# Kernel optimization log

Hardware: AMD Instinct MI355X
Metric: run time of the kernel (lower is better)

Reference implementation:

```python
import jax, jax.numpy as jnp
import numpy as np

B, K, V, D, H, S, KS = 4, 4, 32, 64, 4, 1024, 5
GROUPS = K * V  # 128


def setup_inputs() -> dict:
    key = jax.random.key(0)
    k1, k2 = jax.random.split(key, 2)
    x = jax.random.normal(k1, (B, GROUPS * 3, S), dtype=jnp.float32)
    # grouped causal conv weight: (out_ch, in_ch_per_group, ks) = (K*V*D*3, 3, KS)
    W = jax.random.normal(k2, (GROUPS * D * 3, 3, KS), dtype=jnp.float32) * 0.05
    b = jnp.zeros((GROUPS * D * 3,), dtype=jnp.float32)
    return {"x": x, "W": W, "b": b}


def reference(x, W, b):
    temperature = 1.0
    dk = D // H
    # --- TCN (stand-in): causal grouped conv1d, groups = K*V ---
    xp = jnp.pad(x, ((0, 0), (0, 0), (KS - 1, 0)))  # left-pad for causality
    y = jax.lax.conv_general_dilated(
        xp, W, window_strides=(1,), padding='VALID',
        dimension_numbers=('NCH', 'OIH', 'NCH'),
        feature_group_count=GROUPS,
    ) + b[None, :, None]                      # (B, K*V*3*D, S)
    # channel layout per group is (3, D) to mirror torch reshape
    y = y.reshape(B * K, V, 3, D, S)
    q, k, v = y[:, :, 0], y[:, :, 1], y[:, :, 2]   # each (BK, V, D, S)
    q = q.reshape(B * K, V, H, dk, S)
    k = k.reshape(B * K, V, H, dk, S)
    v = v.reshape(B * K, V, H, dk, S)
    scale = (dk ** -0.5) / temperature
    # per-timestep attention over variables: (BK, H, S, Vq, Vk)
    logits = jnp.einsum('bqhds,bkhds->bhsqk', q, k) * scale
    attn = jax.nn.softmax(logits, axis=-1)
    # x_out[b,h,s,q,d] = sum_k attn * v  -> permute(0,3,1,4,2) layout (BK,V,H,dk,S)
    xo = jnp.einsum('bhsqk,bkhds->bqhds', attn, v)
    xo = xo.reshape(B * K, V * D, S).reshape(B, K * V * D, S)
    # mean over heads, to (BK, Vq, Vk, S) then (B, K, V, V, S)
    attn_m = jnp.transpose(attn.mean(axis=1), (0, 2, 3, 1)).reshape(B, K, V, V, S)
    return xo, attn_m
```

## Files before the change

kernel.cpp:

```cpp
#include <hip/hip_runtime.h>
#include <hip/hip_bf16.h>
#include <stdint.h>

#define SCALE 0.25f

typedef __attribute__((ext_vector_type(8))) short bf16x8;
typedef __attribute__((ext_vector_type(4))) float f32x4;
typedef __attribute__((ext_vector_type(16))) float f32x16;

__global__ __launch_bounds__(256) void prep_w2_kernel(const float* __restrict__ W,
                                                      float* __restrict__ W2) {
    int idx = blockIdx.x * 256 + threadIdx.x;
    int o = idx >> 4, j = idx & 15;
    W2[idx] = (j < 15) ? W[o * 15 + j] : 0.f;
}

#define XS_OFF 0
#define QK0_OFF 6912
#define QK1_OFF 23296
#define VT0_OFF 39680
#define VT1_OFF 49920
#define PT_OFF 60160
#define RING_OFF 80640
#define LDS_TOTAL 162880

__global__ __launch_bounds__(512) void fused4_kernel(const float* __restrict__ x,
                                                     const float* __restrict__ W2,
                                                     const float* __restrict__ bias,
                                                     float* __restrict__ out,
                                                     float* __restrict__ out_am) {
    extern __shared__ char smraw[];
    _Float16* xs = (_Float16*)(smraw + XS_OFF);
    unsigned short* pT = (unsigned short*)(smraw + PT_OFF);
    float* xo = (float*)(smraw + RING_OFF);
    float* att = (float*)smraw;

    int bi = blockIdx.x, slot = bi & 7, jj = bi >> 3;
    int k_ = slot >> 1, b = jj >> 4, st = ((slot & 1) << 4) | (jj & 15);
    int bk = b * 4 + k_;

    int t = threadIdx.x;
    int wid = t >> 6, lane = t & 63;
    int l31 = lane & 31, hi2 = lane >> 5;
    int l15 = lane & 15, hi4 = lane >> 4;

    int v = t >> 4, dk = t & 15;
    int g3 = (k_ * 32 + v) * 3;

    float w[3][16], bs[3];
    auto loadw = [&](int hh) {
        #pragma unroll
        for (int c3 = 0; c3 < 3; ++c3) {
            int row = (g3 + c3) * 64 + hh * 16 + dk;
            const float4* p = (const float4*)(W2 + (size_t)row * 16);
            float4 a0 = p[0], a1 = p[1], a2 = p[2], a3 = p[3];
            w[c3][0] = a0.x;  w[c3][1] = a0.y;  w[c3][2] = a0.z;  w[c3][3] = a0.w;
            w[c3][4] = a1.x;  w[c3][5] = a1.y;  w[c3][6] = a1.z;  w[c3][7] = a1.w;
            w[c3][8] = a2.x;  w[c3][9] = a2.y;  w[c3][10] = a2.z; w[c3][11] = a2.w;
            w[c3][12] = a3.x; w[c3][13] = a3.y; w[c3][14] = a3.z; w[c3][15] = a3.w;
            bs[c3] = bias[row];
        }
    };

    auto conv_stage = [&](int qs, int bufi) {
        __hip_bfloat16* qk = (__hip_bfloat16*)(smraw + (bufi ? QK1_OFF : QK0_OFF));
        __hip_bfloat16* vt = (__hip_bfloat16*)(smraw + (bufi ? VT1_OFF : VT0_OFF));
        float xw[3][12];
        #pragma unroll
        for (int i = 0; i < 3; ++i)
            #pragma unroll
            for (int j = 0; j < 12; ++j)
                xw[i][j] = (float)xs[(v * 3 + i) * 36 + qs * 8 + j];
        #pragma unroll
        for (int s8 = 0; s8 < 8; ++s8) {
            float a0 = bs[0], a1 = bs[1], a2 = bs[2];
            #pragma unroll
            for (int i = 0; i < 3; ++i)
                #pragma unroll
                for (int tt = 0; tt < 5; ++tt) {
                    float xv = xw[i][s8 + tt];
                    a0 = fmaf(xv, w[0][i * 5 + tt], a0);
                    a1 = fmaf(xv, w[1][i * 5 + tt], a1);
                    a2 = fmaf(xv, w[2][i * 5 + tt], a2);
                }
            qk[(s8 * 2 + 0) * 512 + v * 16 + dk] = __float2bfloat16(a0);
            qk[(s8 * 2 + 1) * 512 + v * 16 + dk] = __float2bfloat16(a1);
            vt[(s8 * 16 + dk) * 40 + v] = __float2bfloat16(a2);
        }
    };

    auto sweep = [&](int hp) {
        int rb = (32 * hp) % 40;
        int u = t >> 3;
        int s4 = (t & 7) * 4;
        #pragma unroll
        for (int j = 0; j < 8; ++j) {
            int c_loc = j * 64 + u;
            int col = c_loc ^ (4 * ((c_loc >> 4) & 7));
            float4 o;
            #pragma unroll
            for (int i2 = 0; i2 < 4; ++i2) {
                int r = rb + s4 + i2; if (r >= 40) r -= 40;
                (&o.x)[i2] = xo[r * 514 + col];
            }
            int qv = c_loc >> 4, dkc = c_loc & 15;
            int c = k_ * 2048 + qv * 64 + hp * 16 + dkc;
            *(float4*)(out + ((size_t)b * 8192 + c) * 1024 + st * 32 + s4) = o;
        }
    };

    float acc_am[4][16];
    #pragma unroll
    for (int a = 0; a < 4; ++a)
        #pragma unroll
        for (int r = 0; r < 16; ++r) acc_am[a][r] = 0.f;

    loadw(0);
    {
        int sbase = st * 32 - 4;
        #pragma unroll
        for (int i = 0; i < 7; ++i) {
            int idx = i * 512 + t;
            if (idx < 3456) {
                int row = idx / 36, col = idx - row * 36;
                int sg = sbase + col;
                float val = (sg >= 0) ? x[((size_t)b * 384 + k_ * 96 + row) * 1024 + sg] : 0.f;
                xs[idx] = (_Float16)val;
            }
        }
    }
    __syncthreads();
    conv_stage(0, 0);
    __syncthreads();

    for (int h = 0; h < 4; ++h) {
        #pragma unroll
        for (int q = 0; q < 4; ++q) {
            if (q == 3 && h < 3) loadw(h + 1);

            {
                const __hip_bfloat16* qk =
                    (const __hip_bfloat16*)(smraw + ((q & 1) ? QK1_OFF : QK0_OFF));
                const __hip_bfloat16* vt =
                    (const __hip_bfloat16*)(smraw + ((q & 1) ? VT1_OFF : VT0_OFF));
                const __hip_bfloat16* qb = qk + (wid * 2) * 512 + l31 * 16 + hi2 * 8;
                bf16x8 qf = *(const bf16x8*)qb;
                bf16x8 kf = *(const bf16x8*)(qb + 512);

                f32x16 zc;
                #pragma unroll
                for (int i = 0; i < 16; ++i) zc[i] = 0.f;
                f32x16 lg = __builtin_amdgcn_mfma_f32_32x32x16_bf16(kf, qf, zc, 0, 0, 0);

                float p[16], m = -3.0e38f;
                #pragma unroll
                for (int r = 0; r < 16; ++r) { p[r] = lg[r] * SCALE; m = fmaxf(m, p[r]); }
                m = fmaxf(m, __shfl_xor(m, 32));
                float ssum = 0.f;
                #pragma unroll
                for (int r = 0; r < 16; ++r) { p[r] = __expf(p[r] - m); ssum += p[r]; }
                ssum += __shfl_xor(ssum, 32);
                float inv = 1.f / ssum;
                #pragma unroll
                for (int r = 0; r < 16; ++r) { p[r] *= inv; acc_am[q][r] += p[r]; }

                unsigned* pTrow = (unsigned*)(pT + (size_t)(wid * 32 + l31) * 40);
                int wsw = (l31 >> 3) & 1 ? 4 : 0;
                #pragma unroll
                for (int mm = 0; mm < 8; ++mm) {
                    unsigned pk;
                    asm("v_cvt_pk_bf16_f32 %0, %1, %2"
                        : "=v"(pk) : "v"(p[2 * mm]), "v"(p[2 * mm + 1]));
                    pTrow[((mm & 1) + 4 * (mm >> 1) + 2 * hi2) ^ wsw] = pk;
                }

                int rsw = (l15 >> 3) & 1 ? 8 : 0;
                bf16x8 vf = *(const bf16x8*)&vt[(wid * 16 + l15) * 40 + hi4 * 8];
                bf16x8 p1 = *(const bf16x8*)&pT[(wid * 32 + l15) * 40 + (hi4 * 8 ^ rsw)];
                bf16x8 p2 = *(const bf16x8*)&pT[(wid * 32 + 16 + l15) * 40 + (hi4 * 8 ^ rsw)];
                f32x4 z4;
                #pragma unroll
                for (int i = 0; i < 4; ++i) z4[i] = 0.f;
                f32x4 xo1 = __builtin_amdgcn_mfma_f32_16x16x32_bf16(vf, p1, z4, 0, 0, 0);
                f32x4 xo2 = __builtin_amdgcn_mfma_f32_16x16x32_bf16(vf, p2, z4, 0, 0, 0);

                int rr = (32 * h + 8 * q + wid) % 40;
                float* row = xo + rr * 514;
                int sw = 4 * (l15 & 7);
                *(f32x4*)(row + ((l15 * 16 + hi4 * 4) ^ sw)) = xo1;
                *(f32x4*)(row + (((16 + l15) * 16 + hi4 * 4) ^ sw)) = xo2;
            }

            if (!(h == 3 && q == 3)) {
                conv_stage((q + 1) & 3, (q + 1) & 1);
            }

            if (q == 0 && h > 0) sweep(h - 1);

            __syncthreads();
        }
    }
    sweep(3);
    __syncthreads();

    #pragma unroll
    for (int pass = 0; pass < 2; ++pass) {
        if (pass) __syncthreads();
        if ((l31 >> 4) == pass) {
            int qh = l31 & 15;
            int csw = 4 * (qh & 7);
            #pragma unroll
            for (int q = 0; q < 4; ++q) {
                int sp = q * 8 + wid;
                int colp = sp ^ csw;
                #pragma unroll
                for (int r = 0; r < 16; ++r) {
                    int kv = (r & 3) + 8 * (r >> 2) + 4 * hi2;
                    att[(qh * 32 + kv) * 36 + colp] = 0.25f * acc_am[q][r];
                }
            }
        }
        __syncthreads();
        #pragma unroll
        for (int j = 0; j < 8; ++j) {
            int tr = j * 64 + (t >> 3);
            int csw = 4 * ((tr >> 5) & 7);
            int s4 = (t & 7) * 4;
            float4 o;
            o.x = att[tr * 36 + ((s4 + 0) ^ csw)];
            o.y = att[tr * 36 + ((s4 + 1) ^ csw)];
            o.z = att[tr * 36 + ((s4 + 2) ^ csw)];
            o.w = att[tr * 36 + ((s4 + 3) ^ csw)];
            *(float4*)(out_am + ((size_t)bk * 1024 + pass * 512 + tr) * 1024 + st * 32 + s4) = o;
        }
    }
}

extern "C" void kernel_launch(void* const* d_in, const int* in_sizes, int n_in,
                              void* d_out, int out_size, void* d_ws, size_t ws_size,
                              hipStream_t stream) {
    const float* x = (const float*)d_in[0];
    const float* W = (const float*)d_in[1];
    const float* bias = (const float*)d_in[2];
    float* out = (float*)d_out;
    float* out_am = out + (size_t)33554432;

    float* W2 = (float*)d_ws;

    (void)hipFuncSetAttribute((const void*)fused4_kernel,
                              hipFuncAttributeMaxDynamicSharedMemorySize, LDS_TOTAL);

    prep_w2_kernel<<<1536, 256, 0, stream>>>(W, W2);
    fused4_kernel<<<512, 512, LDS_TOTAL, stream>>>(x, W2, bias, out, out_am);
}
```

Before: 142.4 us.

## Use fp16 dot2 conv, register-held xo output, fp16 attn-mean accumulators

Reworks the fused kernel in several ways. Conv weights and inputs are packed as fp16 pairs and the conv uses v_dot2 instructions instead of scalar fp32 FMAs. The LDS ring buffer for the attention output is dropped: MFMA results are kept in registers across the four q sub-steps and written straight to global memory. The attention-mean accumulators move from fp32 to packed fp16. Together these roughly halve LDS usage, with a launch bound that targets higher occupancy, at the cost of reduced precision in the conv and the head-mean accumulation.

```diff
diff --git a/kernel.cpp b/kernel.cpp
--- a/kernel.cpp
+++ b/kernel.cpp
@@ -7,113 +7,139 @@
 typedef __attribute__((ext_vector_type(8))) short bf16x8;
 typedef __attribute__((ext_vector_type(4))) float f32x4;
 typedef __attribute__((ext_vector_type(16))) float f32x16;
-
-__global__ __launch_bounds__(256) void prep_w2_kernel(const float* __restrict__ W,
-                                                      float* __restrict__ W2) {
+typedef _Float16 h2 __attribute__((ext_vector_type(2)));
+typedef unsigned int u32;
+
+static __device__ __forceinline__ float fdot2f(u32 a, u32 b, float c) {
+#if __has_builtin(__builtin_amdgcn_fdot2)
+    return __builtin_amdgcn_fdot2(__builtin_bit_cast(h2, a), __builtin_bit_cast(h2, b), c, false);
+#else
+    h2 ha = __builtin_bit_cast(h2, a), hb = __builtin_bit_cast(h2, b);
+    return c + (float)ha[0] * (float)hb[0] + (float)ha[1] * (float)hb[1];
+#endif
+}
+static __device__ __forceinline__ float lo16f(u32 u) { return (float)__builtin_bit_cast(h2, u)[0]; }
+static __device__ __forceinline__ float hi16f(u32 u) { return (float)__builtin_bit_cast(h2, u)[1]; }
+
+__global__ __launch_bounds__(256) void prep_w3_kernel(const float* __restrict__ W,
+                                                      const float* __restrict__ bias,
+                                                      u32* __restrict__ W3) {
     int idx = blockIdx.x * 256 + threadIdx.x;
-    int o = idx >> 4, j = idx & 15;
-    W2[idx] = (j < 15) ? W[o * 15 + j] : 0.f;
-}
-
-#define XS_OFF 0
-#define QK0_OFF 6912
-#define QK1_OFF 23296
-#define VT0_OFF 39680
-#define VT1_OFF 49920
-#define PT_OFF 60160
-#define RING_OFF 80640
-#define LDS_TOTAL 162880
-
-__global__ __launch_bounds__(512) void fused4_kernel(const float* __restrict__ x,
-                                                     const float* __restrict__ W2,
-                                                     const float* __restrict__ bias,
-                                                     float* __restrict__ out,
-                                                     float* __restrict__ out_am) {
+    if (idx >= 24576 * 12) return;
+    int o = idx / 12, s = idx - o * 12;
+    u32 val = 0;
+    if (s < 9) {
+        int i = s / 3, pp = s - i * 3;
+        float w0 = W[o * 15 + i * 5 + 2 * pp];
+        float w1 = (2 * pp + 1 < 5) ? W[o * 15 + i * 5 + 2 * pp + 1] : 0.f;
+        h2 pk; pk[0] = (_Float16)w0; pk[1] = (_Float16)w1;
+        val = __builtin_bit_cast(u32, pk);
+    } else if (s == 9) {
+        val = __builtin_bit_cast(u32, bias[o]);
+    }
+    W3[idx] = val;
+}
+
+#define QK0_OFF 0
+#define QK1_OFF 16384
+#define VT0_OFF 32768
+#define VT1_OFF 43008
+#define PT_OFF  53248
+#define XS_OFF  73728
+#define LDS_TOTAL 80640
+
+__global__ __launch_bounds__(512, 4) void fused5_kernel(const float* __restrict__ x,
+                                                        const u32* __restrict__ W3,
+                                                        float* __restrict__ out,
+                                                        float* __restrict__ out_am) {
     extern __shared__ char smraw[];
     _Float16* xs = (_Float16*)(smraw + XS_OFF);
     unsigned short* pT = (unsigned short*)(smraw + PT_OFF);
-    float* xo = (float*)(smraw + RING_OFF);
     float* att = (float*)smraw;
 
-    int bi = blockIdx.x, slot = bi & 7, jj = bi >> 3;
-    int k_ = slot >> 1, b = jj >> 4, st = ((slot & 1) << 4) | (jj & 15);
+    int bi = blockIdx.x, slot = bi & 7, jj2 = bi >> 3;
+    int k_ = slot >> 1, b = jj2 >> 4, st = ((slot & 1) << 4) | (jj2 & 15);
     int bk = b * 4 + k_;
 
     int t = threadIdx.x;
     int wid = t >> 6, lane = t & 63;
     int l31 = lane & 31, hi2 = lane >> 5;
     int l15 = lane & 15, hi4 = lane >> 4;
-
     int v = t >> 4, dk = t & 15;
     int g3 = (k_ * 32 + v) * 3;
 
-    float w[3][16], bs[3];
+    u32 WE[3][9]; float bs[3];
     auto loadw = [&](int hh) {
         #pragma unroll
         for (int c3 = 0; c3 < 3; ++c3) {
-            int row = (g3 + c3) * 64 + hh * 16 + dk;
-            const float4* p = (const float4*)(W2 + (size_t)row * 16);
-            float4 a0 = p[0], a1 = p[1], a2 = p[2], a3 = p[3];
-            w[c3][0] = a0.x;  w[c3][1] = a0.y;  w[c3][2] = a0.z;  w[c3][3] = a0.w;
-            w[c3][4] = a1.x;  w[c3][5] = a1.y;  w[c3][6] = a1.z;  w[c3][7] = a1.w;
-            w[c3][8] = a2.x;  w[c3][9] = a2.y;  w[c3][10] = a2.z; w[c3][11] = a2.w;
-            w[c3][12] = a3.x; w[c3][13] = a3.y; w[c3][14] = a3.z; w[c3][15] = a3.w;
-            bs[c3] = bias[row];
+            const uint4* p = (const uint4*)(W3 + (size_t)((g3 + c3) * 64 + hh * 16 + dk) * 12);
+            uint4 A = p[0], B4 = p[1], C4 = p[2];
+            WE[c3][0] = A.x;  WE[c3][1] = A.y;  WE[c3][2] = A.z;  WE[c3][3] = A.w;
+            WE[c3][4] = B4.x; WE[c3][5] = B4.y; WE[c3][6] = B4.z; WE[c3][7] = B4.w;
+            WE[c3][8] = C4.x; bs[c3] = __builtin_bit_cast(float, C4.y);
         }
     };
 
     auto conv_stage = [&](int qs, int bufi) {
-        __hip_bfloat16* qk = (__hip_bfloat16*)(smraw + (bufi ? QK1_OFF : QK0_OFF));
-        __hip_bfloat16* vt = (__hip_bfloat16*)(smraw + (bufi ? VT1_OFF : VT0_OFF));
-        float xw[3][12];
-        #pragma unroll
-        for (int i = 0; i < 3; ++i)
-            #pragma unroll
-            for (int j = 0; j < 12; ++j)
-                xw[i][j] = (float)xs[(v * 3 + i) * 36 + qs * 8 + j];
-        #pragma unroll
-        for (int s8 = 0; s8 < 8; ++s8) {
-            float a0 = bs[0], a1 = bs[1], a2 = bs[2];
-            #pragma unroll
-            for (int i = 0; i < 3; ++i)
-                #pragma unroll
-                for (int tt = 0; tt < 5; ++tt) {
-                    float xv = xw[i][s8 + tt];
-                    a0 = fmaf(xv, w[0][i * 5 + tt], a0);
-                    a1 = fmaf(xv, w[1][i * 5 + tt], a1);
-                    a2 = fmaf(xv, w[2][i * 5 + tt], a2);
-                }
-            qk[(s8 * 2 + 0) * 512 + v * 16 + dk] = __float2bfloat16(a0);
-            qk[(s8 * 2 + 1) * 512 + v * 16 + dk] = __float2bfloat16(a1);
-            vt[(s8 * 16 + dk) * 40 + v] = __float2bfloat16(a2);
+        __hip_bfloat16* qkw = (__hip_bfloat16*)(smraw + (bufi ? QK1_OFF : QK0_OFF));
+        __hip_bfloat16* vtw = (__hip_bfloat16*)(smraw + (bufi ? VT1_OFF : VT0_OFF));
+        const int PI_ = qs & 1;
+        #pragma unroll
+        for (int hb = 0; hb < 2; ++hb) {
+            float acc0[4], acc1[4], acc2[4];
+            #pragma unroll
+            for (int j4 = 0; j4 < 4; ++j4) { acc0[j4] = bs[0]; acc1[j4] = bs[1]; acc2[j4] = bs[2]; }
+            #pragma unroll
+            for (int ii = 0; ii < 3; ++ii) {
+                const u32* xrow = (const u32*)xs + (v * 3 + ii) * 18 + 8 * hb + ((qs - PI_) >> 1);
+                u32 Dv[9];
+                #pragma unroll
+                for (int d = 0; d < 9; ++d) Dv[d] = xrow[d];
+                u32 wp0[3], wp1[3]; float wsc[3];
+                #pragma unroll
+                for (int c3 = 0; c3 < 3; ++c3) {
+                    if (PI_) {
+                        wp0[c3] = __builtin_amdgcn_alignbit(WE[c3][ii * 3 + 1], WE[c3][ii * 3 + 0], 16);
+                        wp1[c3] = __builtin_amdgcn_alignbit(WE[c3][ii * 3 + 2], WE[c3][ii * 3 + 1], 16);
+                        wsc[c3] = lo16f(WE[c3][ii * 3 + 0]);
+                    } else {
+                        wp0[c3] = WE[c3][ii * 3 + 0];
+                        wp1[c3] = WE[c3][ii * 3 + 1];
+                        wsc[c3] = lo16f(WE[c3][ii * 3 + 2]);
+                    }
+                }
+                #pragma unroll
+                for (int j4 = 0; j4 < 4; ++j4) {
+                    u32 pa = Dv[2 * j4 + PI_], pb = Dv[2 * j4 + 1 + PI_];
+                    float xsc = PI_ ? hi16f(Dv[2 * j4]) : lo16f(Dv[2 * j4 + 2]);
+                    acc0[j4] = fdot2f(wp0[0], pa, acc0[j4]);
+                    acc0[j4] = fdot2f(wp1[0], pb, acc0[j4]);
+                    acc0[j4] = fmaf(wsc[0], xsc, acc0[j4]);
+                    acc1[j4] = fdot2f(wp0[1], pa, acc1[j4]);
+                    acc1[j4] = fdot2f(wp1[1], pb, acc1[j4]);
+                    acc1[j4] = fmaf(wsc[1], xsc, acc1[j4]);
+                    acc2[j4] = fdot2f(wp0[2], pa, acc2[j4]);
+                    acc2[j4] = fdot2f(wp1[2], pb, acc2[j4]);
+                    acc2[j4] = fmaf(wsc[2], xsc, acc2[j4]);
+                }
+            }
+            #pragma unroll
+            for (int j4 = 0; j4 < 4; ++j4) {
+                int j_ = hb * 4 + j4;
+                qkw[(j_ * 2 + 0) * 512 + v * 16 + dk] = __float2bfloat16(acc0[j4]);
+                qkw[(j_ * 2 + 1) * 512 + v * 16 + dk] = __float2bfloat16(acc1[j4]);
+                vtw[(j_ * 16 + dk) * 40 + v] = __float2bfloat16(acc2[j4]);
+            }
         }
     };
 
-    auto sweep = [&](int hp) {
-        int rb = (32 * hp) % 40;
-        int u = t >> 3;
-        int s4 = (t & 7) * 4;
-        #pragma unroll
-        for (int j = 0; j < 8; ++j) {
-            int c_loc = j * 64 + u;
-            int col = c_loc ^ (4 * ((c_loc >> 4) & 7));
-            float4 o;
-            #pragma unroll
-            for (int i2 = 0; i2 < 4; ++i2) {
-                int r = rb + s4 + i2; if (r >= 40) r -= 40;
-                (&o.x)[i2] = xo[r * 514 + col];
-            }
-            int qv = c_loc >> 4, dkc = c_loc & 15;
-            int c = k_ * 2048 + qv * 64 + hp * 16 + dkc;
-            *(float4*)(out + ((size_t)b * 8192 + c) * 1024 + st * 32 + s4) = o;
-        }
-    };
-
-    float acc_am[4][16];
+    h2 quart; quart[0] = (_Float16)0.25f; quart[1] = (_Float16)0.25f;
+    h2 accQ[4][8];
     #pragma unroll
     for (int a = 0; a < 4; ++a)
         #pragma unroll
-        for (int r = 0; r < 16; ++r) acc_am[a][r] = 0.f;
+        for (int m = 0; m < 8; ++m) { accQ[a][m][0] = (_Float16)0.f; accQ[a][m][1] = (_Float16)0.f; }
+    f32x4 xo_acc[4][2];
 
     loadw(0);
     {
@@ -162,7 +188,7 @@
                 ssum += __shfl_xor(ssum, 32);
                 float inv = 1.f / ssum;
                 #pragma unroll
-                for (int r = 0; r < 16; ++r) { p[r] *= inv; acc_am[q][r] += p[r]; }
+                for (int r = 0; r < 16; ++r) p[r] *= inv;
 
                 unsigned* pTrow = (unsigned*)(pT + (size_t)(wid * 32 + l31) * 40);
                 int wsw = (l31 >> 3) & 1 ? 4 : 0;
@@ -172,36 +198,43 @@
                     asm("v_cvt_pk_bf16_f32 %0, %1, %2"
                         : "=v"(pk) : "v"(p[2 * mm]), "v"(p[2 * mm + 1]));
                     pTrow[((mm & 1) + 4 * (mm >> 1) + 2 * hi2) ^ wsw] = pk;
+                    h2 pk2 = __builtin_bit_cast(h2, __builtin_amdgcn_cvt_pkrtz(p[2 * mm], p[2 * mm + 1]));
+                    accQ[q][mm] += pk2 * quart;
                 }
 
                 int rsw = (l15 >> 3) & 1 ? 8 : 0;
-                bf16x8 vf = *(const bf16x8*)&vt[(wid * 16 + l15) * 40 + hi4 * 8];
+                bf16x8 vf = *(const bf16x8*)((const unsigned short*)(vt) + (wid * 16 + l15) * 40 + hi4 * 8);
                 bf16x8 p1 = *(const bf16x8*)&pT[(wid * 32 + l15) * 40 + (hi4 * 8 ^ rsw)];
                 bf16x8 p2 = *(const bf16x8*)&pT[(wid * 32 + 16 + l15) * 40 + (hi4 * 8 ^ rsw)];
                 f32x4 z4;
                 #pragma unroll
                 for (int i = 0; i < 4; ++i) z4[i] = 0.f;
-                f32x4 xo1 = __builtin_amdgcn_mfma_f32_16x16x32_bf16(vf, p1, z4, 0, 0, 0);
-                f32x4 xo2 = __builtin_amdgcn_mfma_f32_16x16x32_bf16(vf, p2, z4, 0, 0, 0);
-
-                int rr = (32 * h + 8 * q + wid) % 40;
-                float* row = xo + rr * 514;
-                int sw = 4 * (l15 & 7);
-                *(f32x4*)(row + ((l15 * 16 + hi4 * 4) ^ sw)) = xo1;
-                *(f32x4*)(row + (((16 + l15) * 16 + hi4 * 4) ^ sw)) = xo2;
+                xo_acc[q][0] = __builtin_amdgcn_mfma_f32_16x16x32_bf16(vf, p1, z4, 0, 0, 0);
+                xo_acc[q][1] = __builtin_amdgcn_mfma_f32_16x16x32_bf16(vf, p2, z4, 0, 0, 0);
+
+                if (q == 3) {
+                    size_t sb = (size_t)st * 32 + 4 * wid;
+                    #pragma unroll
+                    for (int fr = 0; fr < 2; ++fr) {
+                        int qv = fr * 16 + l15;
+                        float* cb = out + ((size_t)b * 8192 + k_ * 2048 + qv * 64 + h * 16 + hi4 * 4) * 1024 + sb;
+                        #pragma unroll
+                        for (int r = 0; r < 4; ++r) {
+                            float4 o4;
+                            o4.x = xo_acc[0][fr][r]; o4.y = xo_acc[1][fr][r];
+                            o4.z = xo_acc[2][fr][r]; o4.w = xo_acc[3][fr][r];
+                            *(float4*)(cb + (size_t)r * 1024) = o4;
+                        }
+                    }
+                }
             }
 
             if (!(h == 3 && q == 3)) {
                 conv_stage((q + 1) & 3, (q + 1) & 1);
             }
-
-            if (q == 0 && h > 0) sweep(h - 1);
-
             __syncthreads();
         }
     }
-    sweep(3);
-    __syncthreads();
 
     #pragma unroll
     for (int pass = 0; pass < 2; ++pass) {
@@ -211,12 +244,13 @@
             int csw = 4 * (qh & 7);
             #pragma unroll
             for (int q = 0; q < 4; ++q) {
-                int sp = q * 8 + wid;
+                int sp = 4 * wid + q;
                 int colp = sp ^ csw;
                 #pragma unroll
-                for (int r = 0; r < 16; ++r) {
-                    int kv = (r & 3) + 8 * (r >> 2) + 4 * hi2;
-                    att[(qh * 32 + kv) * 36 + colp] = 0.25f * acc_am[q][r];
+                for (int mm = 0; mm < 8; ++mm) {
+                    int kv = ((2 * mm) & 3) + 8 * (mm >> 1) + 4 * hi2;
+                    att[(qh * 32 + kv) * 36 + colp] = (float)accQ[q][mm][0];
+                    att[(qh * 32 + kv + 1) * 36 + colp] = (float)accQ[q][mm][1];
                 }
             }
         }
@@ -245,11 +279,11 @@
     float* out = (float*)d_out;
     float* out_am = out + (size_t)33554432;
 
-    float* W2 = (float*)d_ws;
-
-    (void)hipFuncSetAttribute((const void*)fused4_kernel,
+    u32* W3 = (u32*)d_ws;
+
+    (void)hipFuncSetAttribute((const void*)fused5_kernel,
                               hipFuncAttributeMaxDynamicSharedMemorySize, LDS_TOTAL);
 
-    prep_w2_kernel<<<1536, 256, 0, stream>>>(W, W2);
-    fused4_kernel<<<512, 512, LDS_TOTAL, stream>>>(x, W2, bias, out, out_am);
-}
+    prep_w3_kernel<<<1152, 256, 0, stream>>>(W, bias, W3);
+    fused5_kernel<<<512, 512, LDS_TOTAL, stream>>>(x, W3, out, out_am);
+}
```

New measurement: 173.8 us. 1.22x slower.
